# Kernel optimization log

Hardware: AMD Instinct MI355X
Metric: run time of the kernel (lower is better)

The kernel has to match this reference:

```python
import jax, jax.numpy as jnp
import numpy as np

N = 50000
E = 800000
NODE_IN = 64
EDGE_IN = 8
OUT = 1
SAGE_DIMS = [(64, 64), (64, 64), (64, 32), (32, 32)]
EDGE_DIMS = [(8, 64), (64, 64), (64, 32), (32, 32)]


def setup_inputs():
    key = jax.random.key(0)
    keys = iter(jax.random.split(key, 64))
    d = {}
    d["x"] = jax.random.normal(next(keys), (N, NODE_IN), jnp.float32)
    d["dis"] = jax.random.normal(next(keys), (E, EDGE_IN), jnp.float32)
    d["edge_index"] = jax.random.randint(next(keys), (2, E), 0, N, dtype=jnp.int32)
    for i, (fi, fo) in enumerate(SAGE_DIMS):
        d[f"s{i}_wl"] = jax.random.normal(next(keys), (fi, fo), jnp.float32) / np.sqrt(fi).astype(np.float32)
        d[f"s{i}_bl"] = jnp.zeros((fo,), jnp.float32)
        d[f"s{i}_wr"] = jax.random.normal(next(keys), (fi, fo), jnp.float32) / np.sqrt(fi).astype(np.float32)
    for i, (fi, h) in enumerate(EDGE_DIMS):
        d[f"e{i}_w1"] = jax.random.normal(next(keys), (fi, 2 * h), jnp.float32) / np.sqrt(fi).astype(np.float32)
        d[f"e{i}_b1"] = jnp.zeros((2 * h,), jnp.float32)
        d[f"e{i}_w2"] = jax.random.normal(next(keys), (2 * h, h), jnp.float32) / np.sqrt(2 * h).astype(np.float32)
        d[f"e{i}_b2"] = jnp.zeros((h,), jnp.float32)
    d["fc_w"] = jax.random.normal(next(keys), (64, OUT), jnp.float32) / 8.0
    d["fc_b"] = jnp.zeros((OUT,), jnp.float32)
    return d


def _sage(x, row, col, wl, bl, wr):
    # PyG SAGEConv (aggr='mean'): lin_l(mean_{j->i} x_j) + lin_r(x_i); lin_l has bias.
    msg = x[row]  # [E, F] gather of source features
    s = jax.ops.segment_sum(msg, col, num_segments=N)
    cnt = jax.ops.segment_sum(jnp.ones((row.shape[0], 1), x.dtype), col, num_segments=N)
    mean = s / jnp.maximum(cnt, 1.0)  # isolated nodes -> 0 (matches scatter-mean)
    return mean @ wl + bl + x @ wr


def _edge_conv(dis, col, w1, b1, w2, b2):
    # EdgeOnlyConv: add_self_loops with num_nodes=E and zero edge_attr, so the
    # output has E rows; self-loop message = lin(0) = b1 and each segment t gets
    # mean = (sum_{edges->t} lin(dis) + b1) / (deg_in(t) + 1); then lin_update.
    msg = dis @ w1 + b1  # [E, 2h]
    s = jax.ops.segment_sum(msg, col, num_segments=E)
    deg = jax.ops.segment_sum(jnp.ones((col.shape[0], 1), dis.dtype), col, num_segments=E)
    aggr = (s + b1) / (deg + 1.0)
    return aggr @ w2 + b2


def _forward(x, dis, edge_index, sage_params, edge_params, fc_w, fc_b):
    row, col = edge_index[0], edge_index[1]
    h = x
    for wl, bl, wr in sage_params:
        h = jax.nn.leaky_relu(_sage(h, row, col, wl, bl, wr))
    d = dis
    for w1, b1, w2, b2 in edge_params:
        d = jax.nn.leaky_relu(_edge_conv(d, col, w1, b1, w2, b2))
    # dropout is identity at inference
    feats = jnp.concatenate([h[row] * h[col], d], axis=1)  # [E, hidden]
    return feats @ fc_w + fc_b


def reference(x, dis, edge_index, s0_wl, s0_bl, s0_wr, s1_wl, s1_bl, s1_wr, s2_wl, s2_bl, s2_wr, s3_wl, s3_bl, s3_wr, e0_w1, e0_b1, e0_w2, e0_b2, e1_w1, e1_b1, e1_w2, e1_b2, e2_w1, e2_b1, e2_w2, e2_b2, e3_w1, e3_b1, e3_w2, e3_b2, fc_w, fc_b):
    sage_params = [(s0_wl, s0_bl, s0_wr), (s1_wl, s1_bl, s1_wr), (s2_wl, s2_bl, s2_wr), (s3_wl, s3_bl, s3_wr)]
    edge_params = [(e0_w1, e0_b1, e0_w2, e0_b2), (e1_w1, e1_b1, e1_w2, e1_b2), (e2_w1, e2_b1, e2_w2, e2_b2), (e3_w1, e3_b1, e3_w2, e3_b2)]
    return _forward(x, dis, edge_index, sage_params, edge_params, fc_w, fc_b)
```

## Files before the change

kernel.cpp:

```cpp
#include <hip/hip_runtime.h>

#define LRELU(v) ((v) > 0.0f ? (v) : 0.01f * (v))

__device__ __forceinline__ unsigned short f2bf(float f) {
    union { float f; unsigned u; } c;
    c.f = f;
    return (unsigned short)((c.u + 0x7fffu + ((c.u >> 16) & 1)) >> 16);
}
__device__ __forceinline__ float bf_lo(unsigned u) {
    union { unsigned i; float f; } v;
    v.i = u << 16;
    return v.f;
}
__device__ __forceinline__ float bf_hi(unsigned u) {
    union { unsigned i; float f; } v;
    v.i = u & 0xffff0000u;
    return v.f;
}

template <int H2, int HOUT>
__device__ __forceinline__ void w12_body(const float* __restrict__ w1,
                                         const float* __restrict__ w2, float* __restrict__ out,
                                         int i, int o) {
    float s = 0.0f;
// ... 102 lines not shown
            int oo = t - 160;
            float raw = ps[640 + oo] + ps[672 + oo] + ps[704 + oo] + ps[736 + oo];
            cbuf[448 + oo] = raw;
            float c = LRELU(raw + b2_3[oo]);
            c4s[oo] = c;
            cbuf[160 + oo] = c;
        }
        __syncthreads();
        a = 0.0f;
        if (w < 8) {
            int oo = t & 127, g = t >> 7;
#pragma unroll
            for (int j = 0; j < 16; ++j) {
                int f = g * 16 + j;
                a += c1[f] * w1_1[f * 128 + oo];
            }
        } else if (w < 12) {
            int l = t - 512;
            int oo = l & 63, g = l >> 6;
#pragma unroll
            for (int j = 0; j < 16; ++j) {
                int f = g * 16 + j;
                a += c2[f] * w1_2[f * 64 + oo];
            }
        } else {
            int l = t - 768;
            int oo = l & 63, g = l >> 6;
#pragma unroll
            for (int j = 0; j < 8; ++j) {
                int f = g * 8 + j;
                a += c3[f] * w1_3[f * 64 + oo];
            }
        }
        ps[t] = a;
        __syncthreads();
        if (t < 128) {
            u1[t] = ps[t] + ps[t + 128] + ps[t + 256] + ps[t + 384];
        } else if (t < 192) {
            int oo = t - 128;
            u2[oo] = ps[512 + oo] + ps[576 + oo] + ps[640 + oo] + ps[704 + oo];
        } else if (t < 256) {
            int oo = t - 192;
            u3[oo] = ps[768 + oo] + ps[832 + oo] + ps[896 + oo] + ps[960 + oo];
        }
        __syncthreads();
        a = 0.0f;
        if (w < 4) {
            int oo = t & 63, g = t >> 6;
#pragma unroll
            for (int j = 0; j < 32; ++j) {
                int k = g * 32 + j;
                a += u1[k] * w2_1[k * 64 + oo];
            }
        } else if (w < 6) {
            int l = t - 256;
            int oo = l & 31, g = l >> 5;
#pragma unroll
            for (int j = 0; j < 16; ++j) {
                int k = g * 16 + j;
                a += u2[k] * w2_2[k * 32 + oo];
            }
        } else if (w < 8) {
            int l = t - 384;
            int oo = l & 31, g = l >> 5;
#pragma unroll
            for (int j = 0; j < 16; ++j) {
                int k = g * 16 + j;
                a += u3[k] * w2_3[k * 32 + oo];
            }
        }
        ps[t] = a;
        if (w == 8) {
            int l = t - 512;
            float v = (l < 32) ? c4s[l] * fcw[32 + l] : 0.0f;
            v += __shfl_down(v, 16);
            v += __shfl_down(v, 8);
            v += __shfl_down(v, 4);
            v += __shfl_down(v, 2);
            v += __shfl_down(v, 1);
            if (l == 0) cbuf[512] = v;
        }
        __syncthreads();
        if (t < 64) {
            cbuf[320 + t] = cbuf[256 + t] + ps[t] + ps[t + 64] + ps[t + 128] + ps[t + 192];
        } else if (t < 96) {
            int oo = t - 64;
            cbuf[416 + oo] = cbuf[384 + oo] + ps[256 + oo] + ps[288 + oo] + ps[320 + oo] +
                             ps[352 + oo];
        } else if (t < 128) {
            int oo = t - 96;
            cbuf[480 + oo] = cbuf[448 + oo] + ps[384 + oo] + ps[416 + oo] + ps[448 + oo] +
                             ps[480 + oo];
        }
    }
}

__global__ void bucket_scan_k(const int* __restrict__ bpart, int* __restrict__ bbase,
                              int* __restrict__ bwp, int NBUCK, int E, int EB) {
    __shared__ int s[512];
    int tid = threadIdx.x;
    int v = 0;
    if (tid < NBUCK) {
        for (int b = 0; b < EB; ++b) v += bpart[(size_t)b * 512 + tid];
    }
    s[tid] = v;
    __syncthreads();
    for (int off = 1; off < 512; off <<= 1) {
        int t = (tid >= off) ? s[tid - off] : 0;
        __syncthreads();
        s[tid] += t;
        __syncthreads();
    }
    if (tid < NBUCK) {
        int ex = s[tid] - v;
        bbase[tid] = ex;
        bwp[tid] = ex;
    }
    if (tid == 0) bbase[NBUCK] = E;
}

__global__ void bucket_scatter_k(const int* __restrict__ row, const int* __restrict__ col,
                                 int* __restrict__ bwp, int2* __restrict__ tmp, int E) {
    __shared__ int lcnt[512];
    __shared__ int gbase[512];
    int tid = threadIdx.x;
    for (int i = tid; i < 512; i += 1024) lcnt[i] = 0;
    __syncthreads();
    int base = blockIdx.x * 8192;
    int lpos[8], bk[8];
    for (int k = 0; k < 8; ++k) {
        int e = base + k * 1024 + tid;
        if (e < E) {
            int b = col[e] >> 7;
            bk[k] = b;
            lpos[k] = atomicAdd(&lcnt[b], 1);
        } else
            bk[k] = -1;
    }
    __syncthreads();
    for (int i = tid; i < 512; i += 1024) {
        int v = lcnt[i];
        gbase[i] = v ? atomicAdd(&bwp[i], v) : 0;
    }
    __syncthreads();
    for (int k = 0; k < 8; ++k) {
        int e = base + k * 1024 + tid;
        if (e < E) {
            int c = col[e];
            tmp[gbase[bk[k]] + lpos[k]] = make_int2(row[e], ((c & 127) << 25) | e);
        }
    }
}

union __align__(16) CsrGemmSM {
    struct {
        int2 buf[6144];
        int lcnt[128];
        int sscan[128];
        int lwp[128];
    } c;
    float sw[64 * 128];
};

__global__ void csr_gemm0_k(const int2* __restrict__ tmp, const int* __restrict__ bbase,
                            int* __restrict__ rowptr, int* __restrict__ cnt,
                            int* __restrict__ rows, int* __restrict__ eids, int N, int E,
                            int NBUCK, const float* __restrict__ h, const float* __restrict__ wl,
                            const float* __restrict__ wr, const float* __restrict__ bl,
                            unsigned short* __restrict__ hl, float* __restrict__ hr) {
    __shared__ CsrGemmSM sm;
    int tid = threadIdx.x;
    if (blockIdx.x < NBUCK) {
        constexpr int CAP = 6144;
        int b = blockIdx.x;
        int s = bbase[b], e = bbase[b + 1];
        int sz = e - s;
        if (tid < 128) sm.c.lcnt[tid] = 0;
        __syncthreads();
        for (int i = tid; i < sz; i += 256) {
            int2 v = tmp[s + i];
            if (i < CAP) sm.c.buf[i] = v;
            atomicAdd(&sm.c.lcnt[((unsigned)v.y) >> 25], 1);
        }
        __syncthreads();
        if (tid < 128) sm.c.sscan[tid] = sm.c.lcnt[tid];
        __syncthreads();
        for (int off = 1; off < 128; off <<= 1) {
            int t = (tid < 128 && tid >= off) ? sm.c.sscan[tid - off] : 0;
            __syncthreads();
            if (tid < 128) sm.c.sscan[tid] += t;
            __syncthreads();
        }
        if (tid < 128) {
            int ex = sm.c.sscan[tid] - sm.c.lcnt[tid];
            sm.c.lwp[tid] = ex;
            int c = b * 128 + tid;
            if (c < N) {
                rowptr[c] = s + ex;
                cnt[c] = sm.c.lcnt[tid];
                if (c == N - 1) rowptr[N] = E;
            }
        }
        __syncthreads();
        for (int i = tid; i < sz; i += 256) {
            int2 v = (i < CAP) ? sm.c.buf[i] : tmp[s + i];
            int cl = ((unsigned)v.y) >> 25;
            int p = atomicAdd(&sm.c.lwp[cl], 1);
            rows[s + p] = v.x;
            eids[s + p] = v.y & 0x1FFFFFF;
        }
        return;
    }
    float* sw = sm.sw;
    int bx = blockIdx.x - NBUCK;
    int tx = tid & 31, ty = tid >> 5;
    for (int idx = tid; idx < 64 * 64; idx += 256) {
        int f = idx >> 6, o = idx & 63;
        sw[f * 128 + o] = wl[idx];
        sw[f * 128 + 64 + o] = wr[idx];
    }
    __syncthreads();
    int og = tx * 4;
    int base = bx * 32 + ty * 4;
    int ix[4] = {min(base + 0, N - 1), min(base + 1, N - 1), min(base + 2, N - 1),
                 min(base + 3, N - 1)};
    float4 s[4] = {{0.f, 0.f, 0.f, 0.f}, {0.f, 0.f, 0.f, 0.f}, {0.f, 0.f, 0.f, 0.f},
                   {0.f, 0.f, 0.f, 0.f}};
#pragma unroll 2
    for (int f = 0; f < 64; f += 4) {
        float4 w0 = *(const float4*)&sw[(f + 0) * 128 + og];
        float4 w1 = *(const float4*)&sw[(f + 1) * 128 + og];
        float4 w2 = *(const float4*)&sw[(f + 2) * 128 + og];
        float4 w3 = *(const float4*)&sw[(f + 3) * 128 + og];
#pragma unroll
        for (int k = 0; k < 4; ++k) {
            float4 v = *(const float4*)(h + (size_t)ix[k] * 64 + f);
            s[k].x += v.x * w0.x + v.y * w1.x + v.z * w2.x + v.w * w3.x;
            s[k].y += v.x * w0.y + v.y * w1.y + v.z * w2.y + v.w * w3.y;
            s[k].z += v.x * w0.z + v.y * w1.z + v.z * w2.z + v.w * w3.z;
            s[k].w += v.x * w0.w + v.y * w1.w + v.z * w2.w + v.w * w3.w;
        }
    }
    bool isR = og >= 64;
    int oo = isR ? og - 64 : og;
    if (isR) {
        float4 bias = *(const float4*)&bl[oo];
#pragma unroll
        for (int k = 0; k < 4; ++k) {
            int i = base + k;
            if (i < N) {
                float4 r = {s[k].x + bias.x, s[k].y + bias.y, s[k].z + bias.z, s[k].w + bias.w};
                *(float4*)(hr + (size_t)i * 64 + oo) = r;
            }
        }
    } else {
#pragma unroll
        for (int k = 0; k < 4; ++k) {
            int i = base + k;
            if (i < N) {
                unsigned short* d = hl + (size_t)i * 64 + oo;
                *(ushort4*)d = make_ushort4(f2bf(s[k].x), f2bf(s[k].y), f2bf(s[k].z), f2bf(s[k].w));
            }
        }
    }
}

template <int FIN, int FOUT, bool BFL>
__global__ void gemm2_k(const float* __restrict__ h, const float* __restrict__ wl,
                        const float* __restrict__ wr, const float* __restrict__ bl,
                        void* __restrict__ hl, float* __restrict__ hr, int N) {
    constexpr int XT = (2 * FOUT) / 4;
    constexpr int YT = 256 / XT;
    constexpr int NPT = 4;
    constexpr int NPB = YT * NPT;
    __shared__ float sw[FIN * 2 * FOUT];
    int lin = threadIdx.y * XT + threadIdx.x;
    for (int idx = lin; idx < FIN * FOUT; idx += 256) {
        int f = idx / FOUT, o = idx % FOUT;
        sw[f * 2 * FOUT + o] = wl[idx];
        sw[f * 2 * FOUT + FOUT + o] = wr[idx];
    }
    __syncthreads();
    int og = threadIdx.x * 4;
    int base = blockIdx.x * NPB + threadIdx.y * NPT;
    int ix[NPT] = {min(base + 0, N - 1), min(base + 1, N - 1), min(base + 2, N - 1),
                   min(base + 3, N - 1)};
    float4 s[NPT] = {{0.f, 0.f, 0.f, 0.f}, {0.f, 0.f, 0.f, 0.f}, {0.f, 0.f, 0.f, 0.f},
                     {0.f, 0.f, 0.f, 0.f}};
#pragma unroll 2
    for (int f = 0; f < FIN; f += 4) {
        float4 w0 = *(const float4*)&sw[(f + 0) * 2 * FOUT + og];
        float4 w1 = *(const float4*)&sw[(f + 1) * 2 * FOUT + og];
        float4 w2 = *(const float4*)&sw[(f + 2) * 2 * FOUT + og];
        float4 w3 = *(const float4*)&sw[(f + 3) * 2 * FOUT + og];
#pragma unroll
        for (int k = 0; k < NPT; ++k) {
            float4 v = *(const float4*)(h + (size_t)ix[k] * FIN + f);
            s[k].x += v.x * w0.x + v.y * w1.x + v.z * w2.x + v.w * w3.x;
            s[k].y += v.x * w0.y + v.y * w1.y + v.z * w2.y + v.w * w3.y;
            s[k].z += v.x * w0.z + v.y * w1.z + v.z * w2.z + v.w * w3.z;
            s[k].w += v.x * w0.w + v.y * w1.w + v.z * w2.w + v.w * w3.w;
        }
    }
    bool isR = og >= FOUT;
    int oo = isR ? og - FOUT : og;
    if (isR) {
        float4 bias = *(const float4*)&bl[oo];
#pragma unroll
        for (int k = 0; k < NPT; ++k) {
            int i = base + k;
            if (i < N) {
                float4 r = {s[k].x + bias.x, s[k].y + bias.y, s[k].z + bias.z, s[k].w + bias.w};
                *(float4*)(hr + (size_t)i * FOUT + oo) = r;
            }
        }
    } else {
#pragma unroll
        for (int k = 0; k < NPT; ++k) {
            int i = base + k;
            if (i < N) {
                if (BFL) {
                    unsigned short* d = (unsigned short*)hl + (size_t)i * FOUT + oo;
                    *(ushort4*)d =
                        make_ushort4(f2bf(s[k].x), f2bf(s[k].y), f2bf(s[k].z), f2bf(s[k].w));
                } else {
                    *(float4*)((float*)hl + (size_t)i * FOUT + oo) = s[k];
                }
            }
        }
    }
}

__global__ void aggr_fused64_bf_k(const unsigned short* __restrict__ hlb,
                                  const float* __restrict__ hr, const int* __restrict__ rowptr,
                                  const int* __restrict__ rows, float* __restrict__ out, int N) {
    int wave = (blockIdx.x * blockDim.x + threadIdx.x) >> 6;
    int lane = threadIdx.x & 63;
    if (wave >= N) return;
    int u = lane >> 4, f4 = lane & 15;
    int s = rowptr[wave], e = rowptr[wave + 1];
    float4 a = {0.f, 0.f, 0.f, 0.f};
    int p = s + u;
    for (; p + 12 < e; p += 16) {
        int r0 = rows[p], r1 = rows[p + 4], r2 = rows[p + 8], r3 = rows[p + 12];
        uint2 v0 = ((const uint2*)(hlb + (size_t)r0 * 64))[f4];
        uint2 v1 = ((const uint2*)(hlb + (size_t)r1 * 64))[f4];
        uint2 v2 = ((const uint2*)(hlb + (size_t)r2 * 64))[f4];
        uint2 v3 = ((const uint2*)(hlb + (size_t)r3 * 64))[f4];
        a.x += (bf_lo(v0.x) + bf_lo(v1.x)) + (bf_lo(v2.x) + bf_lo(v3.x));
        a.y += (bf_hi(v0.x) + bf_hi(v1.x)) + (bf_hi(v2.x) + bf_hi(v3.x));
        a.z += (bf_lo(v0.y) + bf_lo(v1.y)) + (bf_lo(v2.y) + bf_lo(v3.y));
        a.w += (bf_hi(v0.y) + bf_hi(v1.y)) + (bf_hi(v2.y) + bf_hi(v3.y));
    }
    for (; p + 4 < e; p += 8) {
        int r0 = rows[p], r1 = rows[p + 4];
        uint2 v0 = ((const uint2*)(hlb + (size_t)r0 * 64))[f4];
        uint2 v1 = ((const uint2*)(hlb + (size_t)r1 * 64))[f4];
        a.x += bf_lo(v0.x) + bf_lo(v1.x);
        a.y += bf_hi(v0.x) + bf_hi(v1.x);
        a.z += bf_lo(v0.y) + bf_lo(v1.y);
        a.w += bf_hi(v0.y) + bf_hi(v1.y);
    }
    if (p < e) {
        uint2 v = ((const uint2*)(hlb + (size_t)rows[p] * 64))[f4];
        a.x += bf_lo(v.x); a.y += bf_hi(v.x); a.z += bf_lo(v.y); a.w += bf_hi(v.y);
    }
    a.x += __shfl_down(a.x, 32); a.y += __shfl_down(a.y, 32);
    a.z += __shfl_down(a.z, 32); a.w += __shfl_down(a.w, 32);
    a.x += __shfl_down(a.x, 16); a.y += __shfl_down(a.y, 16);
    a.z += __shfl_down(a.z, 16); a.w += __shfl_down(a.w, 16);
    if (lane < 16) {
        float inv = 1.0f / fmaxf((float)(e - s), 1.0f);
        float4 r = ((const float4*)(hr + (size_t)wave * 64))[f4];
        float4 o;
        o.x = LRELU(a.x * inv + r.x);
        o.y = LRELU(a.y * inv + r.y);
        o.z = LRELU(a.z * inv + r.z);
        o.w = LRELU(a.w * inv + r.w);
        ((float4*)(out + (size_t)wave * 64))[f4] = o;
    }
}

template <bool OUTBF>
__device__ __forceinline__ void aggr32_body(const unsigned short* __restrict__ hlb,
                                            const float* __restrict__ hr,
                                            const int* __restrict__ rowptr,
                                            const int* __restrict__ rows, void* __restrict__ out,
                                            int N, int wave, int lane) {
    if (wave >= N) return;
    int u = lane >> 3, f4 = lane & 7;
    int s = rowptr[wave], e = rowptr[wave + 1];
    float4 a = {0.f, 0.f, 0.f, 0.f};
    int p = s + u;
    for (; p + 8 < e; p += 16) {
        int r0 = rows[p], r1 = rows[p + 8];
        uint2 v0 = ((const uint2*)(hlb + (size_t)r0 * 32))[f4];
        uint2 v1 = ((const uint2*)(hlb + (size_t)r1 * 32))[f4];
        a.x += bf_lo(v0.x) + bf_lo(v1.x);
        a.y += bf_hi(v0.x) + bf_hi(v1.x);
        a.z += bf_lo(v0.y) + bf_lo(v1.y);
        a.w += bf_hi(v0.y) + bf_hi(v1.y);
    }
    if (p < e) {
        uint2 v = ((const uint2*)(hlb + (size_t)rows[p] * 32))[f4];
        a.x += bf_lo(v.x); a.y += bf_hi(v.x); a.z += bf_lo(v.y); a.w += bf_hi(v.y);
    }
    a.x += __shfl_down(a.x, 32); a.y += __shfl_down(a.y, 32);
    a.z += __shfl_down(a.z, 32); a.w += __shfl_down(a.w, 32);
    a.x += __shfl_down(a.x, 16); a.y += __shfl_down(a.y, 16);
    a.z += __shfl_down(a.z, 16); a.w += __shfl_down(a.w, 16);
    a.x += __shfl_down(a.x, 8); a.y += __shfl_down(a.y, 8);
    a.z += __shfl_down(a.z, 8); a.w += __shfl_down(a.w, 8);
    if (lane < 8) {
        float inv = 1.0f / fmaxf((float)(e - s), 1.0f);
        const float4* hp = (const float4*)(hr + (size_t)wave * 32);
        float4 r = hp[f4];
        float4 o;
        o.x = LRELU(a.x * inv + r.x);
        o.y = LRELU(a.y * inv + r.y);
        o.z = LRELU(a.z * inv + r.z);
        o.w = LRELU(a.w * inv + r.w);
        if (OUTBF) {
            unsigned short* d = (unsigned short*)out + (size_t)wave * 32 + f4 * 4;
            *(ushort4*)d = make_ushort4(f2bf(o.x), f2bf(o.y), f2bf(o.z), f2bf(o.w));
        } else {
            ((float4*)((float*)out + (size_t)wave * 32))[f4] = o;
        }
    }
}

template <bool OUTBF>
__global__ void aggr_fused32_bf_k(const unsigned short* __restrict__ hlb,
                                  const float* __restrict__ hr, const int* __restrict__ rowptr,
                                  const int* __restrict__ rows, void* __restrict__ out, int N) {
    int wave = (blockIdx.x * blockDim.x + threadIdx.x) >> 6;
    int lane = threadIdx.x & 63;
    aggr32_body<OUTBF>(hlb, hr, rowptr, rows, out, N, wave, lane);
}

__device__ __forceinline__ void edge_aggr8_body(const float* __restrict__ dis,
                                                const int* __restrict__ rowptr,
                                                const int* __restrict__ eids,
                                                float* __restrict__ sd, float* __restrict__ zbuf,
                                                int N, int wave, int lane) {
    if (wave >= N) return;
    zbuf[(size_t)wave * 64 + lane] = 0.0f;
    int u = lane >> 1, f4 = lane & 1;
    int s = rowptr[wave], e = rowptr[wave + 1];
    float4 a = {0.f, 0.f, 0.f, 0.f};
    for (int p = s + u; p < e; p += 32) {
        const float4* dp = (const float4*)(dis + (size_t)eids[p] * 8);
        float4 v = dp[f4];
        a.x += v.x; a.y += v.y; a.z += v.z; a.w += v.w;
    }
    for (int off = 32; off >= 2; off >>= 1) {
        a.x += __shfl_down(a.x, off); a.y += __shfl_down(a.y, off);
        a.z += __shfl_down(a.z, off); a.w += __shfl_down(a.w, off);
    }
    if (lane < 2) ((float4*)(sd + (size_t)wave * 8))[f4] = a;
}

__global__ void aggr32bf_edge_k(const unsigned short* __restrict__ hlb,
                                const float* __restrict__ hr, const int* __restrict__ rowptr,
                                const int* __restrict__ rows, unsigned short* __restrict__ h3b,
                                const float* __restrict__ dis, const int* __restrict__ eids,
                                float* __restrict__ sd, float* __restrict__ zbuf, int N, int NB) {
    int lane = threadIdx.x & 63;
    if (blockIdx.x < NB) {
        int wave = (blockIdx.x * blockDim.x + threadIdx.x) >> 6;
        aggr32_body<true>(hlb, hr, rowptr, rows, (void*)h3b, N, wave, lane);
    } else {
        int wave = ((blockIdx.x - NB) * blockDim.x + threadIdx.x) >> 6;
        edge_aggr8_body(dis, rowptr, eids, sd, zbuf, N, wave, lane);
    }
}

template <int FIN, int FOUT>
__global__ void edge_compute_scatter_k(const float* __restrict__ sd, const int* __restrict__ cnt,
                                       const float* __restrict__ w12, const float* __restrict__ mw2,
                                       const float* __restrict__ b1w2, const float* __restrict__ b2,
                                       const float* __restrict__ cnext,
                                       const int* __restrict__ col, float* __restrict__ sdnext,
                                       int N, float* __restrict__ zbuf, int zf4) {
    constexpr int ROWS = 256 / FOUT;
    constexpr int NPT = 4;
    constexpr int NPB = ROWS * NPT;
    __shared__ float sw[FIN * FOUT];
    int lin = threadIdx.y * FOUT + threadIdx.x;
    for (int idx = lin; idx < FIN * FOUT; idx += 256) sw[idx] = w12[idx];
    __syncthreads();
    if (zf4) {
        float4 z4 = {0.f, 0.f, 0.f, 0.f};
        for (int z = blockIdx.x * 256 + lin; z < zf4; z += gridDim.x * 256)
            ((float4*)zbuf)[z] = z4;
    }
    int o = threadIdx.x;
    int base = blockIdx.x * NPB + threadIdx.y * NPT;
    int ix[NPT] = {min(base + 0, N - 1), min(base + 1, N - 1), min(base + 2, N - 1),
                   min(base + 3, N - 1)};
    float s[NPT] = {0.f, 0.f, 0.f, 0.f};
#pragma unroll 2
    for (int f = 0; f < FIN; f += 4) {
        float w0 = sw[(f + 0) * FOUT + o], w1 = sw[(f + 1) * FOUT + o];
        float w2 = sw[(f + 2) * FOUT + o], w3 = sw[(f + 3) * FOUT + o];
#pragma unroll
        for (int k = 0; k < NPT; ++k) {
            float4 v = *(const float4*)(sd + (size_t)ix[k] * FIN + f);
            s[k] += v.x * w0 + v.y * w1 + v.z * w2 + v.w * w3;
        }
    }
    float mo = mw2[o], bo = b1w2[o], b2o = b2[o], co = cnext[o];
#pragma unroll
    for (int k = 0; k < NPT; ++k) {
        int i = base + k;
        if (i < N) {
            float deg = (float)cnt[i];
            float inv = 1.0f / (deg + 1.0f);
            float val = LRELU((s[k] + deg * mo + bo) * inv + b2o);
            atomicAdd(&sdnext[(size_t)col[i] * FOUT + o], val - co);
        }
    }
}

__global__ void edge_dot_k(const float* __restrict__ sd, const int* __restrict__ cnt,
                           const float* __restrict__ w12, const float* __restrict__ mw2,
                           const float* __restrict__ b1w2, const float* __restrict__ b2,
                           const float* __restrict__ fcw, float* __restrict__ ddot, int N) {
    constexpr int FIN = 32, FOUT = 32;
    constexpr int NPT = 4;
    constexpr int NPB = (256 / FOUT) * NPT;
    __shared__ float sw[FIN * FOUT];
    int lin = threadIdx.y * FOUT + threadIdx.x;
    for (int idx = lin; idx < FIN * FOUT; idx += 256) sw[idx] = w12[idx];
    __syncthreads();
    int o = threadIdx.x;
    int base = blockIdx.x * NPB + threadIdx.y * NPT;
    int ix[NPT] = {min(base + 0, N - 1), min(base + 1, N - 1), min(base + 2, N - 1),
                   min(base + 3, N - 1)};
    float s[NPT] = {0.f, 0.f, 0.f, 0.f};
#pragma unroll 2
    for (int f = 0; f < FIN; f += 4) {
        float w0 = sw[(f + 0) * FOUT + o], w1 = sw[(f + 1) * FOUT + o];
        float w2 = sw[(f + 2) * FOUT + o], w3 = sw[(f + 3) * FOUT + o];
#pragma unroll
        for (int k = 0; k < NPT; ++k) {
            float4 v = *(const float4*)(sd + (size_t)ix[k] * FIN + f);
            s[k] += v.x * w0 + v.y * w1 + v.z * w2 + v.w * w3;
        }
    }
    float mo = mw2[o], bo = b1w2[o], b2o = b2[o], fw = fcw[32 + o];
#pragma unroll
    for (int k = 0; k < NPT; ++k) {
        float deg = (float)cnt[ix[k]];
        float inv = 1.0f / (deg + 1.0f);
        float v = LRELU((s[k] + deg * mo + bo) * inv + b2o) * fw;
        v += __shfl_down(v, 16);
        v += __shfl_down(v, 8);
        v += __shfl_down(v, 4);
        v += __shfl_down(v, 2);
        v += __shfl_down(v, 1);
        if (o == 0 && base + k < N) ddot[base + k] = v;
    }
}

__global__ void final_csr_k(const unsigned short* __restrict__ h3b,
                            const float* __restrict__ ddot, const float* __restrict__ cbuf,
                            const int* __restrict__ rowptr, const int* __restrict__ rows,
                            const int* __restrict__ eids, const float* __restrict__ fcw,
                            const float* __restrict__ fcb, float* __restrict__ out, int N) {
    int wave = (blockIdx.x * blockDim.x + threadIdx.x) >> 6;
    int lane = threadIdx.x & 63;
    if (wave >= N) return;
    int u = lane >> 3, f4 = lane & 7;
    int s = rowptr[wave], e = rowptr[wave + 1];
    uint2 hc = ((const uint2*)(h3b + (size_t)wave * 32))[f4];
    float c0 = bf_lo(hc.x), c1 = bf_hi(hc.x), c2 = bf_lo(hc.y), c3 = bf_hi(hc.y);
    float4 w = ((const float4*)fcw)[f4];
    float wc0 = c0 * w.x, wc1 = c1 * w.y, wc2 = c2 * w.z, wc3 = c3 * w.w;
    float fb = fcb[0];
    float cdot = cbuf[512];
    int p = s + u;
    for (; p + 8 < e; p += 16) {
        int ra = rows[p], rb = rows[p + 8];
        int ea_ = eids[p], eb_ = eids[p + 8];
        uint2 va = ((const uint2*)(h3b + (size_t)ra * 32))[f4];
        uint2 vb = ((const uint2*)(h3b + (size_t)rb * 32))[f4];
        float ta = bf_lo(va.x) * wc0 + bf_hi(va.x) * wc1 + bf_lo(va.y) * wc2 + bf_hi(va.y) * wc3;
        float tb = bf_lo(vb.x) * wc0 + bf_hi(vb.x) * wc1 + bf_lo(vb.y) * wc2 + bf_hi(vb.y) * wc3;
        ta += __shfl_down(ta, 4); tb += __shfl_down(tb, 4);
        ta += __shfl_down(ta, 2); tb += __shfl_down(tb, 2);
        ta += __shfl_down(ta, 1); tb += __shfl_down(tb, 1);
        if (f4 == 0) {
            out[ea_] = ta + fb + (ea_ < N ? ddot[ea_] : cdot);
            out[eb_] = tb + fb + (eb_ < N ? ddot[eb_] : cdot);
        }
    }
    if (p < e) {
        int ra = rows[p];
        int ea_ = eids[p];
        uint2 va = ((const uint2*)(h3b + (size_t)ra * 32))[f4];
        float ta = bf_lo(va.x) * wc0 + bf_hi(va.x) * wc1 + bf_lo(va.y) * wc2 + bf_hi(va.y) * wc3;
        ta += __shfl_down(ta, 4);
        ta += __shfl_down(ta, 2);
        ta += __shfl_down(ta, 1);
        if (f4 == 0) out[ea_] = ta + fb + (ea_ < N ? ddot[ea_] : cdot);
    }
}

extern "C" void kernel_launch(void* const* d_in, const int* in_sizes, int n_in, void* d_out,
                              int out_size, void* d_ws, size_t ws_size, hipStream_t stream) {
    const float* x = (const float*)d_in[0];
    const float* dis = (const float*)d_in[1];
    const int* ei = (const int*)d_in[2];
    const float* s_wl[4] = {(const float*)d_in[3], (const float*)d_in[6], (const float*)d_in[9],
                            (const float*)d_in[12]};
    const float* s_bl[4] = {(const float*)d_in[4], (const float*)d_in[7], (const float*)d_in[10],
                            (const float*)d_in[13]};
    const float* s_wr[4] = {(const float*)d_in[5], (const float*)d_in[8], (const float*)d_in[11],
                            (const float*)d_in[14]};
    const float* e_w1[4] = {(const float*)d_in[15], (const float*)d_in[19], (const float*)d_in[23],
                            (const float*)d_in[27]};
    const float* e_b1[4] = {(const float*)d_in[16], (const float*)d_in[20], (const float*)d_in[24],
                            (const float*)d_in[28]};
    const float* e_w2[4] = {(const float*)d_in[17], (const float*)d_in[21], (const float*)d_in[25],
                            (const float*)d_in[29]};
    const float* e_b2[4] = {(const float*)d_in[18], (const float*)d_in[22], (const float*)d_in[26],
                            (const float*)d_in[30]};
    const float* fcw = (const float*)d_in[31];
    const float* fcb = (const float*)d_in[32];

    const int N = in_sizes[0] / 64;
    const int E = in_sizes[1] / 8;
    const int* row = ei;
    const int* col = ei + E;
    const int NBUCK = (N + 127) / 128;
    const int EB = (E + 8191) / 8192;

    auto au = [](size_t v) { return (v + 255) & ~(size_t)255; };
    char* p = (char*)d_ws;
    int* cnt = (int*)p;       p += au((size_t)N * 4);
    int* rowptr = (int*)p;    p += au((size_t)(N + 1) * 4);
    int* bbase = (int*)p;     p += au(513 * 4);
    int* bwp = (int*)p;       p += au(512 * 4);
    float* w12_0 = (float*)p; p += au(512 * 4);
    float* w12_1 = (float*)p; p += au(4096 * 4);
    float* w12_2 = (float*)p; p += au(2048 * 4);
    float* w12_3 = (float*)p; p += au(1024 * 4);
    float* cbuf = (float*)p;  p += au(544 * 4);
    int* rowsA = (int*)p;     p += au((size_t)E * 4);
    int* eidsA = (int*)p;     p += au((size_t)E * 4);
    float* acc = (float*)p;   p += au((size_t)N * 64 * 4);
    float* hA = (float*)p;    p += au((size_t)N * 64 * 4);
    float* hB = (float*)p;    p += au((size_t)N * 64 * 4);
    float* dvA = (float*)p;   p += au((size_t)N * 64 * 4);
    float* dvB = (float*)p;   p += au((size_t)N * 64 * 4);

    int2* tmp = (int2*)dvA;
    int* bpart = (int*)hB;
    unsigned short* hlb = (unsigned short*)acc;
    unsigned short* h3b = (unsigned short*)hA;
    float* ddot = dvB;

    const int G0 = (N + 31) / 32;
    const int WPB = 4;
    const int NB = (N + WPB - 1) / WPB;

    count_w12c_k<<<EB + 169, 1024, 0, stream>>>(
        col, bpart, E, EB, e_w1[0], e_w2[0], w12_0, e_w1[1], e_w2[1], w12_1, e_w1[2], e_w2[2],
        w12_2, e_w1[3], e_w2[3], w12_3, e_b1[0], e_b2[0], e_b1[1], e_b2[1], e_b1[2], e_b2[2],
        e_b1[3], e_b2[3], fcw, cbuf);
    bucket_scan_k<<<1, 512, 0, stream>>>(bpart, bbase, bwp, NBUCK, E, EB);
    bucket_scatter_k<<<EB, 1024, 0, stream>>>(row, col, bwp, tmp, E);
    csr_gemm0_k<<<NBUCK + G0, 256, 0, stream>>>(tmp, bbase, rowptr, cnt, rowsA, eidsA, N, E,
                                                NBUCK, x, s_wl[0], s_wr[0], s_bl[0], hlb, dvB);

    aggr_fused64_bf_k<<<NB, 256, 0, stream>>>(hlb, dvB, rowptr, rowsA, hA, N);
    gemm2_k<64, 64, true><<<G0, dim3(32, 8), 0, stream>>>(hA, s_wl[1], s_wr[1], s_bl[1], hlb,
                                                          dvB, N);
    aggr_fused64_bf_k<<<NB, 256, 0, stream>>>(hlb, dvB, rowptr, rowsA, hB, N);
    gemm2_k<64, 32, true><<<(N + 63) / 64, dim3(16, 16), 0, stream>>>(hB, s_wl[2], s_wr[2],
                                                                      s_bl[2], hlb, dvB, N);
    aggr_fused32_bf_k<false><<<NB, 256, 0, stream>>>(hlb, dvB, rowptr, rowsA, hA, N);
    gemm2_k<32, 32, true><<<(N + 63) / 64, dim3(16, 16), 0, stream>>>(hA, s_wl[3], s_wr[3],
                                                                      s_bl[3], hlb, dvB, N);
    aggr32bf_edge_k<<<2 * NB, 256, 0, stream>>>(hlb, dvB, rowptr, rowsA, h3b, dis, eidsA, hB, dvA,
                                                N, NB);

    edge_compute_scatter_k<8, 64><<<(N + 15) / 16, dim3(64, 4), 0, stream>>>(
        hB, cnt, w12_0, cbuf + 192, cbuf + 192, e_b2[0], cbuf + 0, col, dvA, N, acc, N * 16);
    edge_compute_scatter_k<64, 64><<<(N + 15) / 16, dim3(64, 4), 0, stream>>>(
        dvA, cnt, w12_1, cbuf + 320, cbuf + 256, e_b2[1], cbuf + 64, col, acc, N, hB, N * 8);
    edge_compute_scatter_k<64, 32><<<(N + 31) / 32, dim3(32, 8), 0, stream>>>(
        acc, cnt, w12_2, cbuf + 416, cbuf + 384, e_b2[2], cbuf + 128, col, hB, N, nullptr, 0);
    edge_dot_k<<<(N + 31) / 32, dim3(32, 8), 0, stream>>>(hB, cnt, w12_3, cbuf + 480, cbuf + 448,
                                                          e_b2[3], fcw, ddot, N);

    final_csr_k<<<NB, 256, 0, stream>>>(h3b, ddot, cbuf, rowptr, rowsA, eidsA, fcw, fcb,
                                        (float*)d_out, N);
}
```

Baseline: 468.8 us.

## Co-schedule SAGE and edge-conv chains in shared launches via block-range dispatch

Turns the gemm, aggregation and edge-scatter kernels into device-function bodies. Independent stages of the SAGE chain and the edge-conv chain now run in the same launch, with the block index range picking which body a block executes. This cuts the launch count, and small launches can overlap, filling the GPU better. In exchange the workspace gets dedicated buffers instead of aliased ones, so it uses more memory. Mixed blocks also share one shared-memory footprint, which can lower occupancy.

Result: faster. 455.6 us (-2.8%).

```diff
diff --git a/kernel.cpp b/kernel.cpp
--- a/kernel.cpp
+++ b/kernel.cpp
@@ -278,137 +278,26 @@
     }
 }
 
-union __align__(16) CsrGemmSM {
-    struct {
-        int2 buf[6144];
-        int lcnt[128];
-        int sscan[128];
-        int lwp[128];
-    } c;
-    float sw[64 * 128];
-};
-
-__global__ void csr_gemm0_k(const int2* __restrict__ tmp, const int* __restrict__ bbase,
-                            int* __restrict__ rowptr, int* __restrict__ cnt,
-                            int* __restrict__ rows, int* __restrict__ eids, int N, int E,
-                            int NBUCK, const float* __restrict__ h, const float* __restrict__ wl,
-                            const float* __restrict__ wr, const float* __restrict__ bl,
-                            unsigned short* __restrict__ hl, float* __restrict__ hr) {
-    __shared__ CsrGemmSM sm;
-    int tid = threadIdx.x;
-    if (blockIdx.x < NBUCK) {
-        constexpr int CAP = 6144;
-        int b = blockIdx.x;
-        int s = bbase[b], e = bbase[b + 1];
-        int sz = e - s;
-        if (tid < 128) sm.c.lcnt[tid] = 0;
-        __syncthreads();
-        for (int i = tid; i < sz; i += 256) {
-            int2 v = tmp[s + i];
-            if (i < CAP) sm.c.buf[i] = v;
-            atomicAdd(&sm.c.lcnt[((unsigned)v.y) >> 25], 1);
-        }
-        __syncthreads();
-        if (tid < 128) sm.c.sscan[tid] = sm.c.lcnt[tid];
-        __syncthreads();
-        for (int off = 1; off < 128; off <<= 1) {
-            int t = (tid < 128 && tid >= off) ? sm.c.sscan[tid - off] : 0;
-            __syncthreads();
-            if (tid < 128) sm.c.sscan[tid] += t;
-            __syncthreads();
-        }
-        if (tid < 128) {
-            int ex = sm.c.sscan[tid] - sm.c.lcnt[tid];
-            sm.c.lwp[tid] = ex;
-            int c = b * 128 + tid;
-            if (c < N) {
-                rowptr[c] = s + ex;
-                cnt[c] = sm.c.lcnt[tid];
-                if (c == N - 1) rowptr[N] = E;
-            }
-        }
-        __syncthreads();
-        for (int i = tid; i < sz; i += 256) {
-            int2 v = (i < CAP) ? sm.c.buf[i] : tmp[s + i];
-            int cl = ((unsigned)v.y) >> 25;
-            int p = atomicAdd(&sm.c.lwp[cl], 1);
-            rows[s + p] = v.x;
-            eids[s + p] = v.y & 0x1FFFFFF;
-        }
-        return;
-    }
-    float* sw = sm.sw;
-    int bx = blockIdx.x - NBUCK;
-    int tx = tid & 31, ty = tid >> 5;
-    for (int idx = tid; idx < 64 * 64; idx += 256) {
-        int f = idx >> 6, o = idx & 63;
-        sw[f * 128 + o] = wl[idx];
-        sw[f * 128 + 64 + o] = wr[idx];
-    }
-    __syncthreads();
-    int og = tx * 4;
-    int base = bx * 32 + ty * 4;
-    int ix[4] = {min(base + 0, N - 1), min(base + 1, N - 1), min(base + 2, N - 1),
-                 min(base + 3, N - 1)};
-    float4 s[4] = {{0.f, 0.f, 0.f, 0.f}, {0.f, 0.f, 0.f, 0.f}, {0.f, 0.f, 0.f, 0.f},
-                   {0.f, 0.f, 0.f, 0.f}};
-#pragma unroll 2
-    for (int f = 0; f < 64; f += 4) {
-        float4 w0 = *(const float4*)&sw[(f + 0) * 128 + og];
-        float4 w1 = *(const float4*)&sw[(f + 1) * 128 + og];
-        float4 w2 = *(const float4*)&sw[(f + 2) * 128 + og];
-        float4 w3 = *(const float4*)&sw[(f + 3) * 128 + og];
-#pragma unroll
-        for (int k = 0; k < 4; ++k) {
-            float4 v = *(const float4*)(h + (size_t)ix[k] * 64 + f);
-            s[k].x += v.x * w0.x + v.y * w1.x + v.z * w2.x + v.w * w3.x;
-            s[k].y += v.x * w0.y + v.y * w1.y + v.z * w2.y + v.w * w3.y;
-            s[k].z += v.x * w0.z + v.y * w1.z + v.z * w2.z + v.w * w3.z;
-            s[k].w += v.x * w0.w + v.y * w1.w + v.z * w2.w + v.w * w3.w;
-        }
-    }
-    bool isR = og >= 64;
-    int oo = isR ? og - 64 : og;
-    if (isR) {
-        float4 bias = *(const float4*)&bl[oo];
-#pragma unroll
-        for (int k = 0; k < 4; ++k) {
-            int i = base + k;
-            if (i < N) {
-                float4 r = {s[k].x + bias.x, s[k].y + bias.y, s[k].z + bias.z, s[k].w + bias.w};
-                *(float4*)(hr + (size_t)i * 64 + oo) = r;
-            }
-        }
-    } else {
-#pragma unroll
-        for (int k = 0; k < 4; ++k) {
-            int i = base + k;
-            if (i < N) {
-                unsigned short* d = hl + (size_t)i * 64 + oo;
-                *(ushort4*)d = make_ushort4(f2bf(s[k].x), f2bf(s[k].y), f2bf(s[k].z), f2bf(s[k].w));
-            }
-        }
-    }
-}
-
-template <int FIN, int FOUT, bool BFL>
-__global__ void gemm2_k(const float* __restrict__ h, const float* __restrict__ wl,
-                        const float* __restrict__ wr, const float* __restrict__ bl,
-                        void* __restrict__ hl, float* __restrict__ hr, int N) {
+template <int FIN, int FOUT>
+__device__ __forceinline__ void gemm2_body(const float* __restrict__ h,
+                                           const float* __restrict__ wl,
+                                           const float* __restrict__ wr,
+                                           const float* __restrict__ bl,
+                                           unsigned short* __restrict__ hl,
+                                           float* __restrict__ hr, int N, int bx, int tid,
+                                           float* sw) {
     constexpr int XT = (2 * FOUT) / 4;
-    constexpr int YT = 256 / XT;
     constexpr int NPT = 4;
-    constexpr int NPB = YT * NPT;
-    __shared__ float sw[FIN * 2 * FOUT];
-    int lin = threadIdx.y * XT + threadIdx.x;
-    for (int idx = lin; idx < FIN * FOUT; idx += 256) {
+    constexpr int NPB = (256 / XT) * NPT;
+    int tx = tid % XT, ty = tid / XT;
+    for (int idx = tid; idx < FIN * FOUT; idx += 256) {
         int f = idx / FOUT, o = idx % FOUT;
         sw[f * 2 * FOUT + o] = wl[idx];
         sw[f * 2 * FOUT + FOUT + o] = wr[idx];
     }
     __syncthreads();
-    int og = threadIdx.x * 4;
-    int base = blockIdx.x * NPB + threadIdx.y * NPT;
+    int og = tx * 4;
+    int base = bx * NPB + ty * NPT;
     int ix[NPT] = {min(base + 0, N - 1), min(base + 1, N - 1), min(base + 2, N - 1),
                    min(base + 3, N - 1)};
     float4 s[NPT] = {{0.f, 0.f, 0.f, 0.f}, {0.f, 0.f, 0.f, 0.f}, {0.f, 0.f, 0.f, 0.f},
@@ -445,23 +334,18 @@
         for (int k = 0; k < NPT; ++k) {
             int i = base + k;
             if (i < N) {
-                if (BFL) {
-                    unsigned short* d = (unsigned short*)hl + (size_t)i * FOUT + oo;
-                    *(ushort4*)d =
-                        make_ushort4(f2bf(s[k].x), f2bf(s[k].y), f2bf(s[k].z), f2bf(s[k].w));
-                } else {
-                    *(float4*)((float*)hl + (size_t)i * FOUT + oo) = s[k];
-                }
-            }
-        }
-    }
-}
-
-__global__ void aggr_fused64_bf_k(const unsigned short* __restrict__ hlb,
-                                  const float* __restrict__ hr, const int* __restrict__ rowptr,
-                                  const int* __restrict__ rows, float* __restrict__ out, int N) {
-    int wave = (blockIdx.x * blockDim.x + threadIdx.x) >> 6;
-    int lane = threadIdx.x & 63;
+                unsigned short* d = hl + (size_t)i * FOUT + oo;
+                *(ushort4*)d = make_ushort4(f2bf(s[k].x), f2bf(s[k].y), f2bf(s[k].z), f2bf(s[k].w));
+            }
+        }
+    }
+}
+
+__device__ __forceinline__ void aggr64_body(const unsigned short* __restrict__ hlb,
+                                            const float* __restrict__ hr,
+                                            const int* __restrict__ rowptr,
+                                            const int* __restrict__ rows,
+                                            float* __restrict__ out, int N, int wave, int lane) {
     if (wave >= N) return;
     int u = lane >> 4, f4 = lane & 15;
     int s = rowptr[wave], e = rowptr[wave + 1];
@@ -555,15 +439,6 @@
     }
 }
 
-template <bool OUTBF>
-__global__ void aggr_fused32_bf_k(const unsigned short* __restrict__ hlb,
-                                  const float* __restrict__ hr, const int* __restrict__ rowptr,
-                                  const int* __restrict__ rows, void* __restrict__ out, int N) {
-    int wave = (blockIdx.x * blockDim.x + threadIdx.x) >> 6;
-    int lane = threadIdx.x & 63;
-    aggr32_body<OUTBF>(hlb, hr, rowptr, rows, out, N, wave, lane);
-}
-
 __device__ __forceinline__ void edge_aggr8_body(const float* __restrict__ dis,
                                                 const int* __restrict__ rowptr,
                                                 const int* __restrict__ eids,
@@ -586,42 +461,26 @@
     if (lane < 2) ((float4*)(sd + (size_t)wave * 8))[f4] = a;
 }
 
-__global__ void aggr32bf_edge_k(const unsigned short* __restrict__ hlb,
-                                const float* __restrict__ hr, const int* __restrict__ rowptr,
-                                const int* __restrict__ rows, unsigned short* __restrict__ h3b,
-                                const float* __restrict__ dis, const int* __restrict__ eids,
-                                float* __restrict__ sd, float* __restrict__ zbuf, int N, int NB) {
-    int lane = threadIdx.x & 63;
-    if (blockIdx.x < NB) {
-        int wave = (blockIdx.x * blockDim.x + threadIdx.x) >> 6;
-        aggr32_body<true>(hlb, hr, rowptr, rows, (void*)h3b, N, wave, lane);
-    } else {
-        int wave = ((blockIdx.x - NB) * blockDim.x + threadIdx.x) >> 6;
-        edge_aggr8_body(dis, rowptr, eids, sd, zbuf, N, wave, lane);
-    }
-}
-
 template <int FIN, int FOUT>
-__global__ void edge_compute_scatter_k(const float* __restrict__ sd, const int* __restrict__ cnt,
-                                       const float* __restrict__ w12, const float* __restrict__ mw2,
-                                       const float* __restrict__ b1w2, const float* __restrict__ b2,
-                                       const float* __restrict__ cnext,
-                                       const int* __restrict__ col, float* __restrict__ sdnext,
-                                       int N, float* __restrict__ zbuf, int zf4) {
-    constexpr int ROWS = 256 / FOUT;
+__device__ __forceinline__ void esc_body(const float* __restrict__ sd, const int* __restrict__ cnt,
+                                         const float* __restrict__ w12,
+                                         const float* __restrict__ mw2,
+                                         const float* __restrict__ b1w2,
+                                         const float* __restrict__ b2,
+                                         const float* __restrict__ cnext,
+                                         const int* __restrict__ col, float* __restrict__ sdnext,
+                                         int N, float* __restrict__ zbuf, int zf4, int bx,
+                                         int nblk, int tid, float* sw) {
     constexpr int NPT = 4;
-    constexpr int NPB = ROWS * NPT;
-    __shared__ float sw[FIN * FOUT];
-    int lin = threadIdx.y * FOUT + threadIdx.x;
-    for (int idx = lin; idx < FIN * FOUT; idx += 256) sw[idx] = w12[idx];
+    constexpr int NPB = (256 / FOUT) * NPT;
+    int o = tid % FOUT, ty = tid / FOUT;
+    for (int idx = tid; idx < FIN * FOUT; idx += 256) sw[idx] = w12[idx];
     __syncthreads();
     if (zf4) {
         float4 z4 = {0.f, 0.f, 0.f, 0.f};
-        for (int z = blockIdx.x * 256 + lin; z < zf4; z += gridDim.x * 256)
-            ((float4*)zbuf)[z] = z4;
-    }
-    int o = threadIdx.x;
-    int base = blockIdx.x * NPB + threadIdx.y * NPT;
+        for (int z = bx * 256 + tid; z < zf4; z += nblk * 256) ((float4*)zbuf)[z] = z4;
+    }
+    int base = bx * NPB + ty * NPT;
     int ix[NPT] = {min(base + 0, N - 1), min(base + 1, N - 1), min(base + 2, N - 1),
                    min(base + 3, N - 1)};
     float s[NPT] = {0.f, 0.f, 0.f, 0.f};
@@ -648,19 +507,21 @@
     }
 }
 
-__global__ void edge_dot_k(const float* __restrict__ sd, const int* __restrict__ cnt,
-                           const float* __restrict__ w12, const float* __restrict__ mw2,
-                           const float* __restrict__ b1w2, const float* __restrict__ b2,
-                           const float* __restrict__ fcw, float* __restrict__ ddot, int N) {
+__device__ __forceinline__ void edot_body(const float* __restrict__ sd,
+                                          const int* __restrict__ cnt,
+                                          const float* __restrict__ w12,
+                                          const float* __restrict__ mw2,
+                                          const float* __restrict__ b1w2,
+                                          const float* __restrict__ b2,
+                                          const float* __restrict__ fcw, float* __restrict__ ddot,
+                                          int N, int bx, int tid, float* sw) {
     constexpr int FIN = 32, FOUT = 32;
     constexpr int NPT = 4;
     constexpr int NPB = (256 / FOUT) * NPT;
-    __shared__ float sw[FIN * FOUT];
-    int lin = threadIdx.y * FOUT + threadIdx.x;
-    for (int idx = lin; idx < FIN * FOUT; idx += 256) sw[idx] = w12[idx];
+    int o = tid % 32, ty = tid / 32;
+    for (int idx = tid; idx < FIN * FOUT; idx += 256) sw[idx] = w12[idx];
     __syncthreads();
-    int o = threadIdx.x;
-    int base = blockIdx.x * NPB + threadIdx.y * NPT;
+    int base = bx * NPB + ty * NPT;
     int ix[NPT] = {min(base + 0, N - 1), min(base + 1, N - 1), min(base + 2, N - 1),
                    min(base + 3, N - 1)};
     float s[NPT] = {0.f, 0.f, 0.f, 0.f};
@@ -687,6 +548,170 @@
         v += __shfl_down(v, 1);
         if (o == 0 && base + k < N) ddot[base + k] = v;
     }
+}
+
+union __align__(16) CsrGemmSM {
+    struct {
+        int2 buf[6144];
+        int lcnt[128];
+        int sscan[128];
+        int lwp[128];
+    } c;
+    float sw[64 * 128];
+};
+
+__global__ void csr_gemm0_k(const int2* __restrict__ tmp, const int* __restrict__ bbase,
+                            int* __restrict__ rowptr, int* __restrict__ cnt,
+                            int* __restrict__ rows, int* __restrict__ eids, int N, int E,
+                            int NBUCK, const float* __restrict__ h, const float* __restrict__ wl,
+                            const float* __restrict__ wr, const float* __restrict__ bl,
+                            unsigned short* __restrict__ hl, float* __restrict__ hr) {
+    __shared__ CsrGemmSM sm;
+    int tid = threadIdx.x;
+    if (blockIdx.x < NBUCK) {
+        constexpr int CAP = 6144;
+        int b = blockIdx.x;
+        int s = bbase[b], e = bbase[b + 1];
+        int sz = e - s;
+        if (tid < 128) sm.c.lcnt[tid] = 0;
+        __syncthreads();
+        for (int i = tid; i < sz; i += 256) {
+            int2 v = tmp[s + i];
+            if (i < CAP) sm.c.buf[i] = v;
+            atomicAdd(&sm.c.lcnt[((unsigned)v.y) >> 25], 1);
+        }
+        __syncthreads();
+        if (tid < 128) sm.c.sscan[tid] = sm.c.lcnt[tid];
+        __syncthreads();
+        for (int off = 1; off < 128; off <<= 1) {
+            int t = (tid < 128 && tid >= off) ? sm.c.sscan[tid - off] : 0;
+            __syncthreads();
+            if (tid < 128) sm.c.sscan[tid] += t;
+            __syncthreads();
+        }
+        if (tid < 128) {
+            int ex = sm.c.sscan[tid] - sm.c.lcnt[tid];
+            sm.c.lwp[tid] = ex;
+            int c = b * 128 + tid;
+            if (c < N) {
+                rowptr[c] = s + ex;
+                cnt[c] = sm.c.lcnt[tid];
+                if (c == N - 1) rowptr[N] = E;
+            }
+        }
+        __syncthreads();
+        for (int i = tid; i < sz; i += 256) {
+            int2 v = (i < CAP) ? sm.c.buf[i] : tmp[s + i];
+            int cl = ((unsigned)v.y) >> 25;
+            int p = atomicAdd(&sm.c.lwp[cl], 1);
+            rows[s + p] = v.x;
+            eids[s + p] = v.y & 0x1FFFFFF;
+        }
+        return;
+    }
+    gemm2_body<64, 64>(h, wl, wr, bl, hl, hr, N, blockIdx.x - NBUCK, tid, sm.sw);
+}
+
+__global__ void ag64_ea8_k(const unsigned short* __restrict__ hlb, const float* __restrict__ hr,
+                           const int* __restrict__ rowptr, const int* __restrict__ rows,
+                           float* __restrict__ out, const float* __restrict__ dis,
+                           const int* __restrict__ eids, float* __restrict__ sd0,
+                           float* __restrict__ zS1, int N, int NB) {
+    int lane = threadIdx.x & 63;
+    if (blockIdx.x < NB) {
+        int wave = (blockIdx.x * 256 + threadIdx.x) >> 6;
+        aggr64_body(hlb, hr, rowptr, rows, out, N, wave, lane);
+    } else {
+        int wave = ((blockIdx.x - NB) * 256 + threadIdx.x) >> 6;
+        edge_aggr8_body(dis, rowptr, eids, sd0, zS1, N, wave, lane);
+    }
+}
+
+__global__ void g64_esc0_k(const float* __restrict__ h, const float* __restrict__ wl,
+                           const float* __restrict__ wr, const float* __restrict__ bl,
+                           unsigned short* __restrict__ hl, float* __restrict__ hr,
+                           const float* __restrict__ sd0, const int* __restrict__ cnt,
+                           const float* __restrict__ w12, const float* __restrict__ mw2,
+                           const float* __restrict__ b1w2, const float* __restrict__ b2,
+                           const float* __restrict__ cnext, const int* __restrict__ col,
+                           float* __restrict__ S1, float* __restrict__ zS2, int N, int G0,
+                           int E0) {
+    __shared__ float sw[64 * 128];
+    int tid = threadIdx.x;
+    if (blockIdx.x < G0) {
+        gemm2_body<64, 64>(h, wl, wr, bl, hl, hr, N, blockIdx.x, tid, sw);
+    } else {
+        esc_body<8, 64>(sd0, cnt, w12, mw2, b1w2, b2, cnext, col, S1, N, zS2, N * 16,
+                        blockIdx.x - G0, E0, tid, sw);
+    }
+}
+
+__global__ void ag64_esc1_k(const unsigned short* __restrict__ hlb, const float* __restrict__ hr,
+                            const int* __restrict__ rowptr, const int* __restrict__ rows,
+                            float* __restrict__ out, const float* __restrict__ S1,
+                            const int* __restrict__ cnt, const float* __restrict__ w12,
+                            const float* __restrict__ mw2, const float* __restrict__ b1w2,
+                            const float* __restrict__ b2, const float* __restrict__ cnext,
+                            const int* __restrict__ col, float* __restrict__ S2,
+                            float* __restrict__ zS3, int N, int NB, int E0) {
+    __shared__ float sw[64 * 64];
+    int tid = threadIdx.x;
+    if (blockIdx.x < NB) {
+        int wave = (blockIdx.x * 256 + tid) >> 6;
+        aggr64_body(hlb, hr, rowptr, rows, out, N, wave, tid & 63);
+    } else {
+        esc_body<64, 64>(S1, cnt, w12, mw2, b1w2, b2, cnext, col, S2, N, zS3, N * 8,
+                         blockIdx.x - NB, E0, tid, sw);
+    }
+}
+
+__global__ void g32_esc2_k(const float* __restrict__ h, const float* __restrict__ wl,
+                           const float* __restrict__ wr, const float* __restrict__ bl,
+                           unsigned short* __restrict__ hl, float* __restrict__ hr,
+                           const float* __restrict__ S2, const int* __restrict__ cnt,
+                           const float* __restrict__ w12, const float* __restrict__ mw2,
+                           const float* __restrict__ b1w2, const float* __restrict__ b2,
+                           const float* __restrict__ cnext, const int* __restrict__ col,
+                           float* __restrict__ S3, int N, int G2, int E2) {
+    __shared__ float sw[64 * 64];
+    int tid = threadIdx.x;
+    if (blockIdx.x < G2) {
+        gemm2_body<64, 32>(h, wl, wr, bl, hl, hr, N, blockIdx.x, tid, sw);
+    } else {
+        esc_body<64, 32>(S2, cnt, w12, mw2, b1w2, b2, cnext, col, S3, N, nullptr, 0,
+                         blockIdx.x - G2, E2, tid, sw);
+    }
+}
+
+__global__ void ag32_edot_k(const unsigned short* __restrict__ hlb, const float* __restrict__ hr,
+                            const int* __restrict__ rowptr, const int* __restrict__ rows,
+                            float* __restrict__ out, const float* __restrict__ S3,
+                            const int* __restrict__ cnt, const float* __restrict__ w12,
+                            const float* __restrict__ mw2, const float* __restrict__ b1w2,
+                            const float* __restrict__ b2, const float* __restrict__ fcw,
+                            float* __restrict__ ddot, int N, int NB) {
+    __shared__ float sw[32 * 32];
+    int tid = threadIdx.x;
+    if (blockIdx.x < NB) {
+        int wave = (blockIdx.x * 256 + tid) >> 6;
+        aggr32_body<false>(hlb, hr, rowptr, rows, (void*)out, N, wave, tid & 63);
+    } else {
+        edot_body(S3, cnt, w12, mw2, b1w2, b2, fcw, ddot, N, blockIdx.x - NB, tid, sw);
+    }
+}
+
+__global__ void gemm2_32_k(const float* __restrict__ h, const float* __restrict__ wl,
+                           const float* __restrict__ wr, const float* __restrict__ bl,
+                           unsigned short* __restrict__ hl, float* __restrict__ hr, int N) {
+    __shared__ float sw[32 * 64];
+    gemm2_body<32, 32>(h, wl, wr, bl, hl, hr, N, blockIdx.x, threadIdx.x, sw);
+}
+
+__global__ void ag32bf_k(const unsigned short* __restrict__ hlb, const float* __restrict__ hr,
+                         const int* __restrict__ rowptr, const int* __restrict__ rows,
+                         unsigned short* __restrict__ h3b, int N) {
+    int wave = (blockIdx.x * 256 + threadIdx.x) >> 6;
+    aggr32_body<true>(hlb, hr, rowptr, rows, (void*)h3b, N, wave, threadIdx.x & 63);
 }
 
 __global__ void final_csr_k(const unsigned short* __restrict__ h3b,
@@ -764,32 +789,37 @@
 
     auto au = [](size_t v) { return (v + 255) & ~(size_t)255; };
     char* p = (char*)d_ws;
-    int* cnt = (int*)p;       p += au((size_t)N * 4);
-    int* rowptr = (int*)p;    p += au((size_t)(N + 1) * 4);
-    int* bbase = (int*)p;     p += au(513 * 4);
-    int* bwp = (int*)p;       p += au(512 * 4);
-    float* w12_0 = (float*)p; p += au(512 * 4);
-    float* w12_1 = (float*)p; p += au(4096 * 4);
-    float* w12_2 = (float*)p; p += au(2048 * 4);
-    float* w12_3 = (float*)p; p += au(1024 * 4);
-    float* cbuf = (float*)p;  p += au(544 * 4);
-    int* rowsA = (int*)p;     p += au((size_t)E * 4);
-    int* eidsA = (int*)p;     p += au((size_t)E * 4);
-    float* acc = (float*)p;   p += au((size_t)N * 64 * 4);
-    float* hA = (float*)p;    p += au((size_t)N * 64 * 4);
-    float* hB = (float*)p;    p += au((size_t)N * 64 * 4);
-    float* dvA = (float*)p;   p += au((size_t)N * 64 * 4);
-    float* dvB = (float*)p;   p += au((size_t)N * 64 * 4);
-
-    int2* tmp = (int2*)dvA;
-    int* bpart = (int*)hB;
-    unsigned short* hlb = (unsigned short*)acc;
-    unsigned short* h3b = (unsigned short*)hA;
-    float* ddot = dvB;
+    int* cnt = (int*)p;        p += au((size_t)N * 4);
+    int* rowptr = (int*)p;     p += au((size_t)(N + 1) * 4);
+    int* bbase = (int*)p;      p += au(513 * 4);
+    int* bwp = (int*)p;        p += au(512 * 4);
+    float* w12_0 = (float*)p;  p += au(512 * 4);
+    float* w12_1 = (float*)p;  p += au(4096 * 4);
+    float* w12_2 = (float*)p;  p += au(2048 * 4);
+    float* w12_3 = (float*)p;  p += au(1024 * 4);
+    float* cbuf = (float*)p;   p += au(544 * 4);
+    int* bpart = (int*)p;      p += au((size_t)EB * 512 * 4);
+    int* rowsA = (int*)p;      p += au((size_t)E * 4);
+    int* eidsA = (int*)p;      p += au((size_t)E * 4);
+    unsigned short* T = (unsigned short*)p; p += au((size_t)N * 64 * 2);
+    float* R = (float*)p;      p += au((size_t)N * 64 * 4);
+    float* H1 = (float*)p;     p += au((size_t)N * 64 * 4);
+    float* H2 = (float*)p;     p += au((size_t)N * 64 * 4);
+    float* S1 = (float*)p;     p += au((size_t)N * 64 * 4);
+    float* S2 = (float*)p;     p += au((size_t)N * 64 * 4);
+    float* S3 = (float*)p;     p += au((size_t)N * 32 * 4);
+    float* sd0 = (float*)p;    p += au((size_t)N * 8 * 4);
+    unsigned short* h3b = (unsigned short*)p; p += au((size_t)N * 32 * 2);
+    float* ddot = (float*)p;   p += au((size_t)N * 4);
+
+    int2* tmp = (int2*)S1;
 
     const int G0 = (N + 31) / 32;
-    const int WPB = 4;
-    const int NB = (N + WPB - 1) / WPB;
+    const int G2 = (N + 63) / 64;
+    const int G3 = (N + 63) / 64;
+    const int E0 = (N + 15) / 16;
+    const int E2 = (N + 31) / 32;
+    const int NB = (N + 3) / 4;
 
     count_w12c_k<<<EB + 169, 1024, 0, stream>>>(
         col, bpart, E, EB, e_w1[0], e_w2[0], w12_0, e_w1[1], e_w2[1], w12_1, e_w1[2], e_w2[2],
@@ -798,29 +828,21 @@
     bucket_scan_k<<<1, 512, 0, stream>>>(bpart, bbase, bwp, NBUCK, E, EB);
     bucket_scatter_k<<<EB, 1024, 0, stream>>>(row, col, bwp, tmp, E);
     csr_gemm0_k<<<NBUCK + G0, 256, 0, stream>>>(tmp, bbase, rowptr, cnt, rowsA, eidsA, N, E,
-                                                NBUCK, x, s_wl[0], s_wr[0], s_bl[0], hlb, dvB);
-
-    aggr_fused64_bf_k<<<NB, 256, 0, stream>>>(hlb, dvB, rowptr, rowsA, hA, N);
-    gemm2_k<64, 64, true><<<G0, dim3(32, 8), 0, stream>>>(hA, s_wl[1], s_wr[1], s_bl[1], hlb,
-                                                          dvB, N);
-    aggr_fused64_bf_k<<<NB, 256, 0, stream>>>(hlb, dvB, rowptr, rowsA, hB, N);
-    gemm2_k<64, 32, true><<<(N + 63) / 64, dim3(16, 16), 0, stream>>>(hB, s_wl[2], s_wr[2],
-                                                                      s_bl[2], hlb, dvB, N);
-    aggr_fused32_bf_k<false><<<NB, 256, 0, stream>>>(hlb, dvB, rowptr, rowsA, hA, N);
-    gemm2_k<32, 32, true><<<(N + 63) / 64, dim3(16, 16), 0, stream>>>(hA, s_wl[3], s_wr[3],
-                                                                      s_bl[3], hlb, dvB, N);
-    aggr32bf_edge_k<<<2 * NB, 256, 0, stream>>>(hlb, dvB, rowptr, rowsA, h3b, dis, eidsA, hB, dvA,
-                                                N, NB);
-
-    edge_compute_scatter_k<8, 64><<<(N + 15) / 16, dim3(64, 4), 0, stream>>>(
-        hB, cnt, w12_0, cbuf + 192, cbuf + 192, e_b2[0], cbuf + 0, col, dvA, N, acc, N * 16);
-    edge_compute_scatter_k<64, 64><<<(N + 15) / 16, dim3(64, 4), 0, stream>>>(
-        dvA, cnt, w12_1, cbuf + 320, cbuf + 256, e_b2[1], cbuf + 64, col, acc, N, hB, N * 8);
-    edge_compute_scatter_k<64, 32><<<(N + 31) / 32, dim3(32, 8), 0, stream>>>(
-        acc, cnt, w12_2, cbuf + 416, cbuf + 384, e_b2[2], cbuf + 128, col, hB, N, nullptr, 0);
-    edge_dot_k<<<(N + 31) / 32, dim3(32, 8), 0, stream>>>(hB, cnt, w12_3, cbuf + 480, cbuf + 448,
-                                                          e_b2[3], fcw, ddot, N);
-
+                                                NBUCK, x, s_wl[0], s_wr[0], s_bl[0], T, R);
+    ag64_ea8_k<<<2 * NB, 256, 0, stream>>>(T, R, rowptr, rowsA, H1, dis, eidsA, sd0, S1, N, NB);
+    g64_esc0_k<<<G0 + E0, 256, 0, stream>>>(H1, s_wl[1], s_wr[1], s_bl[1], T, R, sd0, cnt, w12_0,
+                                            cbuf + 192, cbuf + 192, e_b2[0], cbuf + 0, col, S1,
+                                            S2, N, G0, E0);
+    ag64_esc1_k<<<NB + E0, 256, 0, stream>>>(T, R, rowptr, rowsA, H2, S1, cnt, w12_1, cbuf + 320,
+                                             cbuf + 256, e_b2[1], cbuf + 64, col, S2, S3, N, NB,
+                                             E0);
+    g32_esc2_k<<<G2 + E2, 256, 0, stream>>>(H2, s_wl[2], s_wr[2], s_bl[2], T, R, S2, cnt, w12_2,
+                                            cbuf + 416, cbuf + 384, e_b2[2], cbuf + 128, col, S3,
+                                            N, G2, E2);
+    ag32_edot_k<<<NB + E2, 256, 0, stream>>>(T, R, rowptr, rowsA, H1, S3, cnt, w12_3, cbuf + 480,
+                                             cbuf + 448, e_b2[3], fcw, ddot, N, NB);
+    gemm2_32_k<<<G3, 256, 0, stream>>>(H1, s_wl[3], s_wr[3], s_bl[3], T, R, N);
+    ag32bf_k<<<NB, 256, 0, stream>>>(T, R, rowptr, rowsA, h3b, N);
     final_csr_k<<<NB, 256, 0, stream>>>(h3b, ddot, cbuf, rowptr, rowsA, eidsA, fcw, fcb,
                                         (float*)d_out, N);
 }
```
